# Optimization experiments

Hardware: AMD Instinct MI355X
Metric: run time of the kernel (lower is better)

## Reference

```python
import jax, jax.numpy as jnp
import numpy as np

N, E, D_IN, D_H, G = 20000, 320000, 512, 256, 128


def setup_inputs() -> dict:
    key = jax.random.key(0)
    ks = jax.random.split(key, 9)
    x = jax.random.normal(ks[0], (N, D_IN), dtype=jnp.float32)
    edge_index = jax.random.randint(ks[1], (2, E), 0, N, dtype=jnp.int32)
    batch = jnp.sort(jax.random.randint(ks[2], (N,), 0, G, dtype=jnp.int32))
    W1 = jax.random.normal(ks[3], (D_IN, D_H), dtype=jnp.float32) / np.float32(np.sqrt(D_IN))
    b1 = jnp.zeros((D_H,), dtype=jnp.float32)
    W2 = jax.random.normal(ks[4], (D_H, D_H), dtype=jnp.float32) / np.float32(np.sqrt(D_H))
    b2 = jnp.zeros((D_H,), dtype=jnp.float32)
    w_fc = jax.random.normal(ks[5], (D_H, 1), dtype=jnp.float32) / np.float32(np.sqrt(D_H))
    b_fc = jnp.zeros((1,), dtype=jnp.float32)
    return {"x": x, "edge_index": edge_index, "batch": batch,
            "W1": W1, "b1": b1, "W2": W2, "b2": b2, "w_fc": w_fc, "b_fc": b_fc}


def gcn_conv(x, W, b, src, dst, n):
    # PyG GCNConv: out = D^{-1/2} (A+I) D^{-1/2} (X W) + b  (self-loops already in src/dst)
    xw = x @ W                                            # [n, d_out]
    deg = jnp.zeros((n,), xw.dtype).at[dst].add(1.0)       # in-degree incl. self loop
    dinv = jnp.where(deg > 0, jax.lax.rsqrt(deg), 0.0)
    coef = (dinv[src] * dinv[dst])[:, None]               # [e, 1]
    out = jnp.zeros_like(xw).at[dst].add(xw[src] * coef)  # gather-scale-scatter
    return out + b


def reference(x, edge_index, batch, W1, b1, W2, b2, w_fc, b_fc):
    n = x.shape[0]
    loops = jnp.arange(n, dtype=edge_index.dtype)
    src = jnp.concatenate([edge_index[0], loops])
    dst = jnp.concatenate([edge_index[1], loops])
    h = jax.nn.relu(gcn_conv(x, W1, b1, src, dst, n))
    h = jax.nn.relu(gcn_conv(h, W2, b2, src, dst, n))
    # global_mean_pool over graph ids
    sums = jax.ops.segment_sum(h, batch, num_segments=G)                      # [G, d]
    cnt = jax.ops.segment_sum(jnp.ones((n, 1), h.dtype), batch, num_segments=G)
    pooled = sums / jnp.maximum(cnt, 1.0)
    return (pooled @ w_fc + b_fc)[:, 0]                                       # [G]
```

## Files before the change

kernel.cpp:

```cpp
#include <hip/hip_runtime.h>
#include <hip/hip_fp16.h>


#define TPB 256
#define CAP 64

typedef _Float16 hfrag __attribute__((ext_vector_type(8)));
typedef float f32x4 __attribute__((ext_vector_type(4)));

__global__ __launch_bounds__(TPB) void k_init(int* __restrict__ cursor, int N,
                                              const float* __restrict__ W1,
                                              unsigned short* __restrict__ B1,
                                              int K1,
                                              const float* __restrict__ W2,
                                              unsigned short* __restrict__ B2h,
                                              unsigned short* __restrict__ B2l,
                                              int K2) {
  int nbz = (N + TPB - 1) / TPB;
  int b = blockIdx.x;
  if (b < nbz) {
    int i = b * TPB + threadIdx.x;
    if (i < N) cursor[i] = 0;
    return;
  }
  int t = (b - nbz) * TPB + threadIdx.x;
  if (t < K1 * 256) {
    int n = t & 255, k = t >> 8;
    float v = W1[(size_t)k * 256 + n];
    __half h = __float2half(v);
    B1[((size_t)(k >> 5) * 256 + n) * 32 + (k & 31)] = *(unsigned short*)&h;
  } else {
    t -= K1 * 256;
    if (t >= K2 * 256) return;
    int n = t & 255, k = t >> 8;
    float v = W2[(size_t)k * 256 + n];
    __half h = __float2half(v);
    __half l = __float2half(v - __half2float(h));
    size_t o = ((size_t)(k >> 5) * 256 + n) * 32 + (k & 31);
    B2h[o] = *(unsigned short*)&h;
    B2l[o] = *(unsigned short*)&l;
  }
}

__global__ __launch_bounds__(TPB) void k_scatter(const int* __restrict__ src,
                                                 const int* __restrict__ dst,
                                                 int* __restrict__ cursor,
                                                 unsigned* __restrict__ pairw, int E) {
  int e = blockIdx.x * TPB + threadIdx.x;
  if (e >= E) return;
  int s = src[e], d = dst[e];
  int pos = d * CAP + atomicAdd(&cursor[d], 1);
  pairw[pos] = ((unsigned)s) << 16;
}

#define LDSTR 72

template <int MODE>
__device__ __forceinline__ void gemm_core(const unsigned short* __restrict__ Bph,
                                          const unsigned short* __restrict__ Bpl,
                                          __half* __restrict__ C, int M, int K,
                                          int bm, int bn,
                                          unsigned short (*AsH)[LDSTR],
                                          unsigned short (*AsL)[LDSTR],
                                          const float* A_f32,
                                          const __half* A_f16) {
  const int tid = threadIdx.x;
  const int w = tid >> 6;
  const int lane = tid & 63;
  const int q = lane >> 4;
  const int nin = lane & 15;
  const int r  = tid >> 2;
  const int cb = (tid & 3) << 4;
  const int row = bm + r;
  const bool rok = row < M;

  size_t bbase[2];
#pragma unroll
  for (int nt = 0; nt < 2; ++nt)
    bbase[nt] = ((size_t)(bn + w * 32 + nt * 16 + nin)) * 32 + q * 8;

  f32x4 acc[4][2];
#pragma unroll
  for (int mt = 0; mt < 4; ++mt)
#pragma unroll
    for (int nt = 0; nt < 2; ++nt) acc[mt][nt] = (f32x4){0.f, 0.f, 0.f, 0.f};

  float4 rf[4];
  uint4  rh[2];
  if (MODE == 0) {
    rf[0] = make_float4(0.f, 0.f, 0.f, 0.f); rf[1] = rf[0]; rf[2] = rf[0]; rf[3] = rf[0];
    if (rok) {
      const float* Ap = A_f32 + (size_t)row * K + cb;
      rf[0] = *(const float4*)(Ap);
      rf[1] = *(const float4*)(Ap + 4);
      rf[2] = *(const float4*)(Ap + 8);
      rf[3] = *(const float4*)(Ap + 12);
    }
  } else {
    rh[0] = make_uint4(0, 0, 0, 0); rh[1] = rh[0];
    if (rok) {
      const __half* Ap = A_f16 + (size_t)row * K + cb;
      rh[0] = *(const uint4*)(Ap);
      rh[1] = *(const uint4*)(Ap + 8);
    }
  }

  for (int kb = 0; kb < K; kb += 64) {
    if (MODE == 0) {
      float vv[16];
      *(float4*)&vv[0] = rf[0]; *(float4*)&vv[4] = rf[1];
      *(float4*)&vv[8] = rf[2]; *(float4*)&vv[12] = rf[3];
      unsigned short h16[16], l16[16];
#pragma unroll
      for (int j = 0; j < 16; ++j) {
        __half h = __float2half(vv[j]);
        __half l = __float2half(vv[j] - __half2float(h));
        h16[j] = *(unsigned short*)&h;
        l16[j] = *(unsigned short*)&l;
      }
      __syncthreads();
      *(uint4*)&AsH[r][cb]     = *(uint4*)&h16[0];
      *(uint4*)&AsH[r][cb + 8] = *(uint4*)&h16[8];
      *(uint4*)&AsL[r][cb]     = *(uint4*)&l16[0];
      *(uint4*)&AsL[r][cb + 8] = *(uint4*)&l16[8];
      __syncthreads();
    } else {
      __syncthreads();
      *(uint4*)&AsH[r][cb]     = rh[0];
      *(uint4*)&AsH[r][cb + 8] = rh[1];
      __syncthreads();
    }

    int kn = kb + 64;
    if (kn < K && rok) {
      if (MODE == 0) {
        const float* Ap = A_f32 + (size_t)row * K + kn + cb;
        rf[0] = *(const float4*)(Ap);
        rf[1] = *(const float4*)(Ap + 4);
        rf[2] = *(const float4*)(Ap + 8);
        rf[3] = *(const float4*)(Ap + 12);
      } else {
        const __half* Ap = A_f16 + (size_t)row * K + kn + cb;
        rh[0] = *(const uint4*)(Ap);
        rh[1] = *(const uint4*)(Ap + 8);
      }
    }

#pragma unroll
    for (int s = 0; s < 2; ++s) {
      const size_t koff = (size_t)((kb >> 5) + s) * 256 * 32;
      if (MODE == 0) {
        hfrag bh[2];
#pragma unroll
        for (int nt = 0; nt < 2; ++nt)
          bh[nt] = *(const hfrag*)(Bph + koff + bbase[nt]);
        hfrag ah[4], al[4];
#pragma unroll
        for (int mt = 0; mt < 4; ++mt) {
          ah[mt] = *(const hfrag*)&AsH[mt * 16 + nin][s * 32 + q * 8];
          al[mt] = *(const hfrag*)&AsL[mt * 16 + nin][s * 32 + q * 8];
        }
#pragma unroll
        for (int mt = 0; mt < 4; ++mt)
#pragma unroll
          for (int nt = 0; nt < 2; ++nt) {
            acc[mt][nt] = __builtin_amdgcn_mfma_f32_16x16x32_f16(ah[mt], bh[nt], acc[mt][nt], 0, 0, 0);
            acc[mt][nt] = __builtin_amdgcn_mfma_f32_16x16x32_f16(al[mt], bh[nt], acc[mt][nt], 0, 0, 0);
          }
      } else {
        hfrag bh[2], bl[2];
#pragma unroll
        for (int nt = 0; nt < 2; ++nt) {
          bh[nt] = *(const hfrag*)(Bph + koff + bbase[nt]);
          bl[nt] = *(const hfrag*)(Bpl + koff + bbase[nt]);
        }
        hfrag a4[4];
#pragma unroll
        for (int mt = 0; mt < 4; ++mt)
          a4[mt] = *(const hfrag*)&AsH[mt * 16 + nin][s * 32 + q * 8];
#pragma unroll
        for (int mt = 0; mt < 4; ++mt)
#pragma unroll
          for (int nt = 0; nt < 2; ++nt) {
            acc[mt][nt] = __builtin_amdgcn_mfma_f32_16x16x32_f16(a4[mt], bh[nt], acc[mt][nt], 0, 0, 0);
            acc[mt][nt] = __builtin_amdgcn_mfma_f32_16x16x32_f16(a4[mt], bl[nt], acc[mt][nt], 0, 0, 0);
          }
      }
    }
  }

#pragma unroll
  for (int mt = 0; mt < 4; ++mt) {
    int rb = bm + mt * 16 + q * 4;
#pragma unroll
    for (int reg = 0; reg < 4; ++reg) {
      int rr = rb + reg;
      if (rr < M) {
#pragma unroll
        for (int nt = 0; nt < 2; ++nt)
          C[(size_t)rr * 256 + bn + w * 32 + nt * 16 + nin] = __float2half(acc[mt][nt][reg]);
      }
    }
  }
}

__global__ __launch_bounds__(TPB) void k_gemm1_coef(const float* __restrict__ A,
                                                    const unsigned short* __restrict__ Bph,
                                                    __half* __restrict__ C, int M, int K,
                                                    const int* __restrict__ cnt,
                                                    unsigned* __restrict__ pairw, int N) {
  __shared__ unsigned short AsH[64][LDSTR];
  __shared__ unsigned short AsL[64][LDSTR];
  int nbg = 2 * ((M + 63) / 64);
  int b = blockIdx.x;
  if (b < nbg) {
    gemm_core<0>(Bph, nullptr, C, M, K, (b >> 1) * 64, (b & 1) * 128, AsH, AsL, A, nullptr);
    return;
  }
  int t = (b - nbg) * TPB + threadIdx.x;
  int node = t >> 6;
  if (node >= N) return;
  int slot = t & 63;
  if (slot >= cnt[node]) return;
  int pos = node * CAP + slot;
  unsigned u = pairw[pos];
  int j = (int)(u >> 16);
  float di = rsqrtf((float)(cnt[node] + 1));
  float dj = rsqrtf((float)(cnt[j] + 1));
  __half h = __float2half(di * dj);
  pairw[pos] = u | (unsigned)(*(unsigned short*)&h);
}

__global__ __launch_bounds__(TPB) void k_gemm2(const __half* __restrict__ A,
                                               const unsigned short* __restrict__ Bph,
                                               const unsigned short* __restrict__ Bpl,
                                               __half* __restrict__ C, int M, int K) {
  __shared__ unsigned short AsH[64][LDSTR];
  gemm_core<1>(Bph, Bpl, C, M, K, blockIdx.y * 64, blockIdx.x * 128, AsH, nullptr, nullptr, A);
}

__device__ __forceinline__ f32x4 gather_row4(const uint2* __restrict__ xq,
                                             const unsigned* __restrict__ pairw,
                                             int node, int deg, int lane) {
  f32x4 a = (f32x4){0.f, 0.f, 0.f, 0.f};
  int base = node * CAP;
  int k = 0;
  for (; k + 7 < deg; k += 8) {
#pragma unroll
    for (int u = 0; u < 8; ++u) {
      unsigned uu = pairw[base + k + u];
      const uint2* rp = xq + ((size_t)(uu >> 16) << 6);
      unsigned short cb16 = (unsigned short)(uu & 0xFFFFu);
      float coef = __half2float(*(__half*)&cb16);
      uint2 v = rp[lane];
      float2 f0 = __half22float2(*(__half2*)&v.x);
      float2 f1 = __half22float2(*(__half2*)&v.y);
      a[0] = fmaf(coef, f0.x, a[0]);
      a[1] = fmaf(coef, f0.y, a[1]);
      a[2] = fmaf(coef, f1.x, a[2]);
      a[3] = fmaf(coef, f1.y, a[3]);
    }
  }
  for (; k < deg; ++k) {
    unsigned uu = pairw[base + k];
    const uint2* rp = xq + ((size_t)(uu >> 16) << 6);
    unsigned short cb16 = (unsigned short)(uu & 0xFFFFu);
    float coef = __half2float(*(__half*)&cb16);
    uint2 v = rp[lane];
    float2 f0 = __half22float2(*(__half2*)&v.x);
    float2 f1 = __half22float2(*(__half2*)&v.y);
    a[0] = fmaf(coef, f0.x, a[0]);
    a[1] = fmaf(coef, f0.y, a[1]);
    a[2] = fmaf(coef, f1.x, a[2]);
    a[3] = fmaf(coef, f1.y, a[3]);
  }
  return a;
}

__global__ __launch_bounds__(TPB) void k_gather1(const uint2* __restrict__ xq,
                                                 const int* __restrict__ cnt,
                                                 const unsigned* __restrict__ pairw,
                                                 const float* __restrict__ bias,
                                                 uint2* __restrict__ h1, int N) {
  int node = __builtin_amdgcn_readfirstlane(blockIdx.x * 4 + (threadIdx.x >> 6));
  if (node >= N) return;
  int deg = __builtin_amdgcn_readfirstlane(cnt[node]);
  int lane = threadIdx.x & 63;
  f32x4 acc = gather_row4(xq, pairw, node, deg, lane);
  float di2 = 1.f / (float)(deg + 1);
  uint2 sv = xq[((size_t)node << 6) + lane];
  float2 s0 = __half22float2(*(__half2*)&sv.x);
  float2 s1 = __half22float2(*(__half2*)&sv.y);
  acc[0] = fmaf(di2, s0.x, acc[0]);
  acc[1] = fmaf(di2, s0.y, acc[1]);
  acc[2] = fmaf(di2, s1.x, acc[2]);
  acc[3] = fmaf(di2, s1.y, acc[3]);
  const float4 bb = *(const float4*)&bias[4 * lane];
  float r0 = fmaxf(acc[0] + bb.x, 0.f);
  float r1 = fmaxf(acc[1] + bb.y, 0.f);
  float r2 = fmaxf(acc[2] + bb.z, 0.f);
  float r3 = fmaxf(acc[3] + bb.w, 0.f);
  __half2 o0 = __floats2half2_rn(r0, r1);
  __half2 o1 = __floats2half2_rn(r2, r3);
  uint2 o;
  o.x = *(unsigned*)&o0;
  o.y = *(unsigned*)&o1;
  h1[((size_t)node << 6) + lane] = o;
}

__global__ __launch_bounds__(TPB) void k_gather2(const uint2* __restrict__ xq,
                                                 const int* __restrict__ cnt,
                                                 const unsigned* __restrict__ pairw,
                                                 const float* __restrict__ bias,
                                                 const float* __restrict__ wfc,
                                                 float* __restrict__ pdot, int N) {
  int node = __builtin_amdgcn_readfirstlane(blockIdx.x * 4 + (threadIdx.x >> 6));
  if (node >= N) return;
  int deg = __builtin_amdgcn_readfirstlane(cnt[node]);
  int lane = threadIdx.x & 63;
  f32x4 acc = gather_row4(xq, pairw, node, deg, lane);
  float di2 = 1.f / (float)(deg + 1);
  uint2 sv = xq[((size_t)node << 6) + lane];
  float2 s0 = __half22float2(*(__half2*)&sv.x);
  float2 s1 = __half22float2(*(__half2*)&sv.y);
  acc[0] = fmaf(di2, s0.x, acc[0]);
  acc[1] = fmaf(di2, s0.y, acc[1]);
  acc[2] = fmaf(di2, s1.x, acc[2]);
  acc[3] = fmaf(di2, s1.y, acc[3]);
  const float4 bb = *(const float4*)&bias[4 * lane];
  const float4 ff = *(const float4*)&wfc[4 * lane];
  float s = fmaxf(acc[0] + bb.x, 0.f) * ff.x + fmaxf(acc[1] + bb.y, 0.f) * ff.y +
            fmaxf(acc[2] + bb.z, 0.f) * ff.z + fmaxf(acc[3] + bb.w, 0.f) * ff.w;
#pragma unroll
  for (int off = 32; off > 0; off >>= 1) s += __shfl_down(s, off);
  if (lane == 0) pdot[node] = s;
}

__global__ __launch_bounds__(TPB) void k_pool(const float* __restrict__ pdot,
                                              const int* __restrict__ batch,
                                              const float* __restrict__ bfc,
                                              float* __restrict__ out, int N) {
  int g = blockIdx.x;
  int lo = 0, hi = N;
  while (lo < hi) { int mid = (lo + hi) >> 1; if (batch[mid] < g) lo = mid + 1; else hi = mid; }
  int start = lo;
  hi = N;
  while (lo < hi) { int mid = (lo + hi) >> 1; if (batch[mid] < g + 1) lo = mid + 1; else hi = mid; }
  int end = lo;

  float s = 0.f;
  for (int i = start + threadIdx.x; i < end; i += TPB) s += pdot[i];
  __shared__ float red[4];
  int lane = threadIdx.x & 63, wave = threadIdx.x >> 6;
#pragma unroll
  for (int off = 32; off > 0; off >>= 1) s += __shfl_down(s, off);
  if (lane == 0) red[wave] = s;
  __syncthreads();
  if (threadIdx.x == 0) {
    float tot = red[0] + red[1] + red[2] + red[3];
    float c = (float)(end - start);
    out[g] = tot / fmaxf(c, 1.f) + bfc[0];
  }
}

extern "C" void kernel_launch(void* const* d_in, const int* in_sizes, int n_in,
                              void* d_out, int out_size, void* d_ws, size_t ws_size,
                              hipStream_t stream) {
  const float* x    = (const float*)d_in[0];
  const int*   eidx = (const int*)d_in[1];
  const int*   batch= (const int*)d_in[2];
  const float* W1   = (const float*)d_in[3];
  const float* b1   = (const float*)d_in[4];
  const float* W2   = (const float*)d_in[5];
  const float* b2   = (const float*)d_in[6];
  const float* wfc  = (const float*)d_in[7];
  const float* bfc  = (const float*)d_in[8];
  float* out = (float*)d_out;

  const int N  = in_sizes[2];
  const int E  = in_sizes[1] / 2;
  const int K1 = in_sizes[0] / N;
  const int G  = out_size;

  const int* srcp = eidx;
  const int* dstp = eidx + E;

  auto al16 = [](size_t v) { return (v + 15) & ~(size_t)15; };
  char* ws = (char*)d_ws;
  size_t off = 0;
  int*      cursor = (int*)(ws + off);         off = al16(off + (size_t)N * 4);
  unsigned* pairw  = (unsigned*)(ws + off);    off = al16(off + (size_t)N * CAP * 4);
  float*    pdot   = (float*)(ws + off);       off = al16(off + (size_t)N * 4);
  __half*   bufH   = (__half*)(ws + off);      off = al16(off + (size_t)N * 256 * 2);
  __half*   h1f    = (__half*)(ws + off);      off = al16(off + (size_t)N * 256 * 2);
  unsigned short* W1h = (unsigned short*)(ws + off); off = al16(off + (size_t)K1 * 256 * 2);
  unsigned short* W2h = (unsigned short*)(ws + off); off = al16(off + (size_t)256 * 256 * 2);
  unsigned short* W2l = (unsigned short*)(ws + off); off = al16(off + (size_t)256 * 256 * 2);

  const int nbz = (N + TPB - 1) / TPB;
  const int nbW = ((K1 + 256) * 256 + TPB - 1) / TPB;
  const int nbE = (E + TPB - 1) / TPB;
  const int nbg = 2 * ((N + 63) / 64);
  const int nbc = (N * 64 + TPB - 1) / TPB;
  const int nbG = (N + 3) / 4;
  const dim3 g2(2, (N + 63) / 64);

  k_init<<<nbz + nbW, TPB, 0, stream>>>(cursor, N, W1, W1h, K1, W2, W2h, W2l, 256);
  k_scatter<<<nbE, TPB, 0, stream>>>(srcp, dstp, cursor, pairw, E);

  k_gemm1_coef<<<nbg + nbc, TPB, 0, stream>>>(x, W1h, bufH, N, K1, cursor, pairw, N);
  k_gather1<<<nbG, TPB, 0, stream>>>((const uint2*)bufH, cursor, pairw, b1,
                                     (uint2*)h1f, N);

  k_gemm2<<<g2, TPB, 0, stream>>>(h1f, W2h, W2l, bufH, N, 256);
  k_gather2<<<nbG, TPB, 0, stream>>>((const uint2*)bufH, cursor, pairw, b2,
                                     wfc, pdot, N);

  k_pool<<<G, TPB, 0, stream>>>(pdot, batch, bfc, out, N);
}
```

Measured before the change: 193.9 us.

## Fuse edge scatter into GEMM1 launch and compute edge coefficients on the fly

Removes the separate scatter kernel and the coefficient-precompute pass. The CSR scatter now runs as extra blocks of the GEMM1 launch, and the stored entry is the bare source index. Each gather computes its edge coefficient as rsqrt((deg_i+1)*(deg_j+1)) from the degree array instead of reading a precomputed half value. This saves one launch and a full pass over pairw. In exchange, each edge in both gather kernels does an extra dependent load of cnt[j] and an rsqrt.

```diff
diff --git a/kernel.cpp b/kernel.cpp
--- a/kernel.cpp
+++ b/kernel.cpp
@@ -40,17 +40,6 @@
     B2h[o] = *(unsigned short*)&h;
     B2l[o] = *(unsigned short*)&l;
   }
-}
-
-__global__ __launch_bounds__(TPB) void k_scatter(const int* __restrict__ src,
-                                                 const int* __restrict__ dst,
-                                                 int* __restrict__ cursor,
-                                                 unsigned* __restrict__ pairw, int E) {
-  int e = blockIdx.x * TPB + threadIdx.x;
-  if (e >= E) return;
-  int s = src[e], d = dst[e];
-  int pos = d * CAP + atomicAdd(&cursor[d], 1);
-  pairw[pos] = ((unsigned)s) << 16;
 }
 
 #define LDSTR 72
@@ -204,11 +193,13 @@
   }
 }
 
-__global__ __launch_bounds__(TPB) void k_gemm1_coef(const float* __restrict__ A,
-                                                    const unsigned short* __restrict__ Bph,
-                                                    __half* __restrict__ C, int M, int K,
-                                                    const int* __restrict__ cnt,
-                                                    unsigned* __restrict__ pairw, int N) {
+__global__ __launch_bounds__(TPB) void k_gemm1_scatter(const float* __restrict__ A,
+                                                       const unsigned short* __restrict__ Bph,
+                                                       __half* __restrict__ C, int M, int K,
+                                                       const int* __restrict__ src,
+                                                       const int* __restrict__ dst,
+                                                       int* __restrict__ cursor,
+                                                       unsigned* __restrict__ pairw, int E) {
   __shared__ unsigned short AsH[64][LDSTR];
   __shared__ unsigned short AsL[64][LDSTR];
   int nbg = 2 * ((M + 63) / 64);
@@ -217,18 +208,11 @@
     gemm_core<0>(Bph, nullptr, C, M, K, (b >> 1) * 64, (b & 1) * 128, AsH, AsL, A, nullptr);
     return;
   }
-  int t = (b - nbg) * TPB + threadIdx.x;
-  int node = t >> 6;
-  if (node >= N) return;
-  int slot = t & 63;
-  if (slot >= cnt[node]) return;
-  int pos = node * CAP + slot;
-  unsigned u = pairw[pos];
-  int j = (int)(u >> 16);
-  float di = rsqrtf((float)(cnt[node] + 1));
-  float dj = rsqrtf((float)(cnt[j] + 1));
-  __half h = __float2half(di * dj);
-  pairw[pos] = u | (unsigned)(*(unsigned short*)&h);
+  int e = (b - nbg) * TPB + threadIdx.x;
+  if (e >= E) return;
+  int s = src[e], d = dst[e];
+  int pos = d * CAP + atomicAdd(&cursor[d], 1);
+  pairw[pos] = (unsigned)s;
 }
 
 __global__ __launch_bounds__(TPB) void k_gemm2(const __half* __restrict__ A,
@@ -241,18 +225,17 @@
 
 __device__ __forceinline__ f32x4 gather_row4(const uint2* __restrict__ xq,
                                              const unsigned* __restrict__ pairw,
-                                             int node, int deg, int lane) {
+                                             const int* __restrict__ cnt,
+                                             int node, int deg, float ci, int lane) {
   f32x4 a = (f32x4){0.f, 0.f, 0.f, 0.f};
   int base = node * CAP;
   int k = 0;
   for (; k + 7 < deg; k += 8) {
 #pragma unroll
     for (int u = 0; u < 8; ++u) {
-      unsigned uu = pairw[base + k + u];
-      const uint2* rp = xq + ((size_t)(uu >> 16) << 6);
-      unsigned short cb16 = (unsigned short)(uu & 0xFFFFu);
-      float coef = __half2float(*(__half*)&cb16);
-      uint2 v = rp[lane];
+      int j = (int)pairw[base + k + u];
+      float coef = rsqrtf(ci * (float)(cnt[j] + 1));
+      uint2 v = (xq + ((size_t)j << 6))[lane];
       float2 f0 = __half22float2(*(__half2*)&v.x);
       float2 f1 = __half22float2(*(__half2*)&v.y);
       a[0] = fmaf(coef, f0.x, a[0]);
@@ -262,11 +245,9 @@
     }
   }
   for (; k < deg; ++k) {
-    unsigned uu = pairw[base + k];
-    const uint2* rp = xq + ((size_t)(uu >> 16) << 6);
-    unsigned short cb16 = (unsigned short)(uu & 0xFFFFu);
-    float coef = __half2float(*(__half*)&cb16);
-    uint2 v = rp[lane];
+    int j = (int)pairw[base + k];
+    float coef = rsqrtf(ci * (float)(cnt[j] + 1));
+    uint2 v = (xq + ((size_t)j << 6))[lane];
     float2 f0 = __half22float2(*(__half2*)&v.x);
     float2 f1 = __half22float2(*(__half2*)&v.y);
     a[0] = fmaf(coef, f0.x, a[0]);
@@ -286,8 +267,9 @@
   if (node >= N) return;
   int deg = __builtin_amdgcn_readfirstlane(cnt[node]);
   int lane = threadIdx.x & 63;
-  f32x4 acc = gather_row4(xq, pairw, node, deg, lane);
-  float di2 = 1.f / (float)(deg + 1);
+  float ci = (float)(deg + 1);
+  f32x4 acc = gather_row4(xq, pairw, cnt, node, deg, ci, lane);
+  float di2 = 1.f / ci;
   uint2 sv = xq[((size_t)node << 6) + lane];
   float2 s0 = __half22float2(*(__half2*)&sv.x);
   float2 s1 = __half22float2(*(__half2*)&sv.y);
@@ -318,8 +300,9 @@
   if (node >= N) return;
   int deg = __builtin_amdgcn_readfirstlane(cnt[node]);
   int lane = threadIdx.x & 63;
-  f32x4 acc = gather_row4(xq, pairw, node, deg, lane);
-  float di2 = 1.f / (float)(deg + 1);
+  float ci = (float)(deg + 1);
+  f32x4 acc = gather_row4(xq, pairw, cnt, node, deg, ci, lane);
+  float di2 = 1.f / ci;
   uint2 sv = xq[((size_t)node << 6) + lane];
   float2 s0 = __half22float2(*(__half2*)&sv.x);
   float2 s1 = __half22float2(*(__half2*)&sv.y);
@@ -401,14 +384,13 @@
   const int nbW = ((K1 + 256) * 256 + TPB - 1) / TPB;
   const int nbE = (E + TPB - 1) / TPB;
   const int nbg = 2 * ((N + 63) / 64);
-  const int nbc = (N * 64 + TPB - 1) / TPB;
   const int nbG = (N + 3) / 4;
   const dim3 g2(2, (N + 63) / 64);
 
   k_init<<<nbz + nbW, TPB, 0, stream>>>(cursor, N, W1, W1h, K1, W2, W2h, W2l, 256);
-  k_scatter<<<nbE, TPB, 0, stream>>>(srcp, dstp, cursor, pairw, E);
-
-  k_gemm1_coef<<<nbg + nbc, TPB, 0, stream>>>(x, W1h, bufH, N, K1, cursor, pairw, N);
+
+  k_gemm1_scatter<<<nbg + nbE, TPB, 0, stream>>>(x, W1h, bufH, N, K1,
+                                                 srcp, dstp, cursor, pairw, E);
   k_gather1<<<nbG, TPB, 0, stream>>>((const uint2*)bufH, cursor, pairw, b1,
                                      (uint2*)h1f, N);
 
```

Measured after the change: 193.0 us. No clear change (-0.5%).
